# Performance work log

Measured on AMD Instinct MI355X. Metric: run time of the kernel, lower is better.

## Reference

```python
import jax, jax.numpy as jnp
import numpy as np

BATCH = 32      # init batch_size
HID = 256       # init hidden_dim
SENT = 64       # sentence_size
WORDS = 64      # words per sentence (the -1 in the view)
N = BATCH * SENT


def setup_inputs() -> dict:
    key = jax.random.key(0)
    k1, k2, k3, k4 = jax.random.split(key, 4)
    stdv_lin = 1.0 / np.sqrt(HID)
    x = jax.random.normal(k1, (N, WORDS, HID), dtype=jnp.float32)
    W = jax.random.uniform(k2, (HID, HID), jnp.float32, -stdv_lin, stdv_lin)
    b = jax.random.uniform(k3, (HID,), jnp.float32, -stdv_lin, stdv_lin)
    context = jax.random.uniform(k4, (HID,), jnp.float32, -stdv_lin, stdv_lin)
    return {"x": x, "W": W, "b": b, "context": context, "sentence_size": SENT}


def reference(x, W, b, context, sentence_size):
    # tanh(Linear(x)) applied per position; vectorized over the batch loop
    attends = jnp.tanh(jnp.einsum("nwh,oh->nwo", x, W) + b)  # [N, WORDS, HID]
    scores = attends * context                                 # [N, WORDS, HID]
    # nn.Softmax on the [-1, HID] view -> softmax over the hidden dim
    alpha = jax.nn.softmax(scores, axis=-1)                    # [N, WORDS, HID]
    attended = x * alpha                                       # legacy same-numel mul
    attended = attended.reshape(BATCH, sentence_size, -1, HID)
    return jnp.sum(attended, axis=2)                           # [BATCH, SENT, HID]
```

## Files before the change

kernel.cpp:

```cpp
#include <hip/hip_runtime.h>
#include <hip/hip_bf16.h>

#define HID 256
#define NROWS 2048
#define NPB 4
#define NHT (NPB * 2)
#define GRID (NROWS / NPB)
#define PITCH 264
#define HTF (32 * 256)

typedef __attribute__((ext_vector_type(8))) short short8;
typedef __attribute__((ext_vector_type(4))) float float4v;
typedef __attribute__((ext_vector_type(4))) unsigned int uint4v;

__device__ __forceinline__ float bf2f(unsigned short u) {
    return __uint_as_float(((unsigned int)u) << 16);
}

__device__ __forceinline__ unsigned int pk_bf16(float a, float b) {
    __hip_bfloat162 p = __float22bfloat162_rn(float2{a, b});
    return *(unsigned int*)&p;
}

__device__ __forceinline__ void bar_sync() {
    __builtin_amdgcn_sched_barrier(0);
    asm volatile("s_waitcnt lgkmcnt(0)");
    __builtin_amdgcn_s_barrier();
    __builtin_amdgcn_sched_barrier(0);
}

__device__ __forceinline__ float row16_sum(float v) {
    float t;
    t = __builtin_bit_cast(float, __builtin_amdgcn_update_dpp(
            0, __builtin_bit_cast(int, v), 0xB1, 0xf, 0xf, true));
    v += t;
    t = __builtin_bit_cast(float, __builtin_amdgcn_update_dpp(
            0, __builtin_bit_cast(int, v), 0x4E, 0xf, 0xf, true));
    v += t;
    t = __builtin_bit_cast(float, __builtin_amdgcn_update_dpp(
            0, __builtin_bit_cast(int, v), 0x124, 0xf, 0xf, true));
    v += t;
    t = __builtin_bit_cast(float, __builtin_amdgcn_update_dpp(
            0, __builtin_bit_cast(int, v), 0x128, 0xf, 0xf, true));
    v += t;
    return v;
}

__global__ __launch_bounds__(512, 4) void attend_fused(
    const float* __restrict__ x, const float* __restrict__ W,
    const float* __restrict__ bias, const float* __restrict__ ctx,
    float* __restrict__ out)
{
    __shared__ unsigned short xs[2][32 * PITCH];
    __shared__ float wsum[8][32];
    __shared__ float rinv[32];

    const int tid  = threadIdx.x;
    const int wave = tid >> 6;
    const int lane = tid & 63;
    const int q    = lane >> 4;
    const int c    = lane & 15;
    const int obase = wave * 32;
    const float* xp = x + (size_t)blockIdx.x * (NPB * 64 * 256);

    float4v R[4];
    {
        const float4v* xv = (const float4v*)xp;
#pragma unroll
        for (int j = 0; j < 4; ++j) R[j] = xv[tid + 512 * j];
    }

    float bb[2], f2[2];
    short8 bfrag[8][2];
#pragma unroll
    for (int nt = 0; nt < 2; ++nt) {
        const int o = obase + 2 * c + nt;
        bb[nt] = bias[o];
        f2[nt] = ctx[o] * 1.4426950408889634f;
        const float* wr = W + (size_t)o * 256 + q * 8;
#pragma unroll
        for (int kt = 0; kt < 8; ++kt) {
            float4v w0 = *(const float4v*)(wr + kt * 32);
            float4v w1 = *(const float4v*)(wr + kt * 32 + 4);
            uint4v u = { pk_bf16(w0.x, w0.y), pk_bf16(w0.z, w0.w),
                         pk_bf16(w1.x, w1.y), pk_bf16(w1.z, w1.w) };
            bfrag[kt][nt] = __builtin_bit_cast(short8, u);
        }
    }

#pragma unroll
    for (int j = 0; j < 4; ++j) {
        const int chunk = tid + 512 * j;
        const int r = chunk >> 6, col4 = (chunk & 63) * 4;
        uint2 u;
        u.x = pk_bf16(R[j].x, R[j].y);
        u.y = pk_bf16(R[j].z, R[j].w);
        *(uint2*)&xs[0][r * PITCH + col4] = u;
    }
    {
        const float4v* xv = (const float4v*)(xp + HTF);
#pragma unroll
        for (int j = 0; j < 4; ++j) R[j] = xv[tid + 512 * j];
    }
    bar_sync();

    float oacc[2] = {0.f, 0.f};
    int cur = 0;
#pragma unroll 1
    for (int h = 0; h < NHT; ++h) {
        const unsigned short* xsc = xs[cur];

        float4v acc[2][2];
#pragma unroll
        for (int mt = 0; mt < 2; ++mt)
#pragma unroll
            for (int nt = 0; nt < 2; ++nt)
                acc[mt][nt] = (float4v){0.f, 0.f, 0.f, 0.f};

#pragma unroll
        for (int kt = 0; kt < 8; ++kt) {
            short8 a[2];
#pragma unroll
            for (int mt = 0; mt < 2; ++mt)
                a[mt] = *(const short8*)&xsc[(mt * 16 + c) * PITCH + kt * 32 + q * 8];
#pragma unroll
            for (int nt = 0; nt < 2; ++nt)
#pragma unroll
                for (int mt = 0; mt < 2; ++mt)
                    acc[mt][nt] = __builtin_amdgcn_mfma_f32_16x16x32_bf16(
                        a[mt], bfrag[kt][nt], acc[mt][nt], 0, 0, 0);
        }

        float psum[2][4];
#pragma unroll
        for (int mt = 0; mt < 2; ++mt)
#pragma unroll
            for (int r = 0; r < 4; ++r)
                psum[mt][r] = 0.f;

#pragma unroll
        for (int nt = 0; nt < 2; ++nt) {
#pragma unroll
            for (int mt = 0; mt < 2; ++mt) {
#pragma unroll
                for (int r = 0; r < 4; ++r) {
                    const float y  = acc[mt][nt][r] + bb[nt];
                    const float E  = __builtin_amdgcn_exp2f(y * 2.8853900817779268f);
                    const float rd = __builtin_amdgcn_rcpf(E + 1.0f);
                    const float t  = __builtin_fmaf(-2.0f, rd, 1.0f);
                    const float e  = __builtin_amdgcn_exp2f(f2[nt] * t);
                    acc[mt][nt][r] = e;
                    psum[mt][r] += e;
                }
            }
        }
#pragma unroll
        for (int mt = 0; mt < 2; ++mt)
#pragma unroll
            for (int r = 0; r < 4; ++r)
                psum[mt][r] = row16_sum(psum[mt][r]);
        if (c == 0) {
#pragma unroll
            for (int mt = 0; mt < 2; ++mt) {
                float4v p = {psum[mt][0], psum[mt][1], psum[mt][2], psum[mt][3]};
                *(float4v*)&wsum[wave][mt * 16 + q * 4] = p;
            }
        }
        bar_sync();
        if (tid < 32) {
            const float t = wsum[0][tid] + wsum[1][tid] + wsum[2][tid] + wsum[3][tid]
                          + wsum[4][tid] + wsum[5][tid] + wsum[6][tid] + wsum[7][tid];
            rinv[tid] = __builtin_amdgcn_rcpf(t);
        }
        bar_sync();

        float ri[2][4];
#pragma unroll
        for (int mt = 0; mt < 2; ++mt)
#pragma unroll
            for (int r = 0; r < 4; ++r)
                ri[mt][r] = rinv[mt * 16 + q * 4 + r];

#pragma unroll
        for (int mt = 0; mt < 2; ++mt) {
#pragma unroll
            for (int r = 0; r < 4; ++r) {
                const int w = mt * 16 + q * 4 + r;
                unsigned int pair = *(const unsigned int*)&xsc[w * PITCH + obase + 2 * c];
                const float wgt = ri[mt][r];
                oacc[0] += bf2f((unsigned short)pair)         * (acc[mt][0][r] * wgt);
                oacc[1] += bf2f((unsigned short)(pair >> 16)) * (acc[mt][1][r] * wgt);
            }
        }
        if (h & 1) {
#pragma unroll
            for (int nt = 0; nt < 2; ++nt) {
                float v = oacc[nt];
                v += __shfl_xor(v, 16);
                v += __shfl_xor(v, 32);
                oacc[nt] = v;
            }
            if (q == 0) {
                const size_t n = (size_t)blockIdx.x * NPB + (h >> 1);
                *(float2*)&out[n * HID + obase + 2 * c] = float2{oacc[0], oacc[1]};
            }
            oacc[0] = 0.f; oacc[1] = 0.f;
        }

        if (h + 1 < NHT) {
#pragma unroll
            for (int j = 0; j < 4; ++j) {
                const int chunk = tid + 512 * j;
                const int r = chunk >> 6, col4 = (chunk & 63) * 4;
                uint2 u;
                u.x = pk_bf16(R[j].x, R[j].y);
                u.y = pk_bf16(R[j].z, R[j].w);
                *(uint2*)&xs[cur ^ 1][r * PITCH + col4] = u;
            }
            if (h + 2 < NHT) {
                const float4v* xv = (const float4v*)(xp + (size_t)(h + 2) * HTF);
#pragma unroll
                for (int j = 0; j < 4; ++j) R[j] = xv[tid + 512 * j];
            }
        }
        bar_sync();
        cur ^= 1;
    }
}

extern "C" void kernel_launch(void* const* d_in, const int* in_sizes, int n_in,
                              void* d_out, int out_size, void* d_ws, size_t ws_size,
                              hipStream_t stream) {
    const float* x    = (const float*)d_in[0];
    const float* W    = (const float*)d_in[1];
    const float* bias = (const float*)d_in[2];
    const float* ctx  = (const float*)d_in[3];
    (void)in_sizes; (void)n_in; (void)d_ws; (void)ws_size;

    attend_fused<<<GRID, 512, 0, stream>>>(x, W, bias, ctx, (float*)d_out);
}
```

Measured before the change: 213.5 us.

## Give each wave a full row with W staged in swizzled shared memory

Each wave now owns one sentence row and computes all 256 outputs, so the softmax over the hidden dim is reduced inside the wave. This removes the cross-wave shared-memory reductions and the block barriers in every step. W is converted to bf16 once per block and stored in an XOR-swizzled 128KB shared buffer. x is held in registers and moved into the accumulator layout with identity-matrix MFMAs instead of a shared-memory round trip. The costs are much higher register and LDS use (two blocks per CU at most), a per-block reload of W, and only 256 blocks in the grid.

```diff
diff --git a/kernel.cpp b/kernel.cpp
--- a/kernel.cpp
+++ b/kernel.cpp
@@ -3,30 +3,15 @@
 
 #define HID 256
 #define NROWS 2048
-#define NPB 4
-#define NHT (NPB * 2)
-#define GRID (NROWS / NPB)
-#define PITCH 264
-#define HTF (32 * 256)
+#define GRID (NROWS / 8)
 
 typedef __attribute__((ext_vector_type(8))) short short8;
 typedef __attribute__((ext_vector_type(4))) float float4v;
 typedef __attribute__((ext_vector_type(4))) unsigned int uint4v;
 
-__device__ __forceinline__ float bf2f(unsigned short u) {
-    return __uint_as_float(((unsigned int)u) << 16);
-}
-
 __device__ __forceinline__ unsigned int pk_bf16(float a, float b) {
     __hip_bfloat162 p = __float22bfloat162_rn(float2{a, b});
     return *(unsigned int*)&p;
-}
-
-__device__ __forceinline__ void bar_sync() {
-    __builtin_amdgcn_sched_barrier(0);
-    asm volatile("s_waitcnt lgkmcnt(0)");
-    __builtin_amdgcn_s_barrier();
-    __builtin_amdgcn_sched_barrier(0);
 }
 
 __device__ __forceinline__ float row16_sum(float v) {
@@ -46,185 +31,150 @@
     return v;
 }
 
-__global__ __launch_bounds__(512, 4) void attend_fused(
+__global__ __launch_bounds__(512, 2) void attend_fused(
     const float* __restrict__ x, const float* __restrict__ W,
     const float* __restrict__ bias, const float* __restrict__ ctx,
     float* __restrict__ out)
 {
-    __shared__ unsigned short xs[2][32 * PITCH];
-    __shared__ float wsum[8][32];
-    __shared__ float rinv[32];
+    __shared__ unsigned short Wb[256 * 256];
 
     const int tid  = threadIdx.x;
     const int wave = tid >> 6;
     const int lane = tid & 63;
     const int q    = lane >> 4;
     const int c    = lane & 15;
-    const int obase = wave * 32;
-    const float* xp = x + (size_t)blockIdx.x * (NPB * 64 * 256);
+    const int n    = blockIdx.x * 8 + wave;
+    const float* xn = x + (size_t)n * (64 * 256);
 
-    float4v R[4];
+    float4v xa[8], xb[8];
     {
-        const float4v* xv = (const float4v*)xp;
+        const float* xr = xn + c * 256 + q * 8;
 #pragma unroll
-        for (int j = 0; j < 4; ++j) R[j] = xv[tid + 512 * j];
+        for (int kt = 0; kt < 8; ++kt) {
+            xa[kt] = *(const float4v*)(xr + kt * 32);
+            xb[kt] = *(const float4v*)(xr + kt * 32 + 4);
+        }
     }
 
-    float bb[2], f2[2];
-    short8 bfrag[8][2];
+    {
+        char* wbb = (char*)Wb;
+#pragma unroll 4
+        for (int i = 0; i < 32; ++i) {
+            const int f4  = tid + 512 * i;
+            const int col = f4 >> 6;
+            const int k4  = (f4 & 63) * 4;
+            float4v v = *((const float4v*)W + f4);
+            uint2 u;
+            u.x = pk_bf16(v.x, v.y);
+            u.y = pk_bf16(v.z, v.w);
+            const int byte = (col * 512 + k4 * 2) ^ ((col & 7) << 4);
+            *(uint2*)(wbb + byte) = u;
+        }
+    }
+
+    float bias16[16], f216[16];
 #pragma unroll
-    for (int nt = 0; nt < 2; ++nt) {
-        const int o = obase + 2 * c + nt;
-        bb[nt] = bias[o];
-        f2[nt] = ctx[o] * 1.4426950408889634f;
-        const float* wr = W + (size_t)o * 256 + q * 8;
+    for (int nt = 0; nt < 16; ++nt) {
+        const int o = nt * 16 + c;
+        bias16[nt] = bias[o];
+        f216[nt]  = ctx[o] * 1.4426950408889634f;
+    }
+
+    short8 ifr[2];
+#pragma unroll
+    for (int p = 0; p < 2; ++p) {
+        short8 f = (short8){0, 0, 0, 0, 0, 0, 0, 0};
+#pragma unroll
+        for (int j = 0; j < 8; ++j)
+            f[j] = (q * 8 + j == p * 16 + c) ? (short)0x3F80 : (short)0;
+        ifr[p] = f;
+    }
+
+    int swzbase[8];
+#pragma unroll
+    for (int kt = 0; kt < 8; ++kt)
+        swzbase[kt] = c * 512 + ((kt * 64 + q * 16) ^ ((c & 7) << 4));
+
+    __syncthreads();
+
+    const char* wbb = (const char*)Wb;
+
+    float oacc[16];
+#pragma unroll
+    for (int nt = 0; nt < 16; ++nt) oacc[nt] = 0.f;
+
+#pragma unroll 1
+    for (int ch = 0; ch < 4; ++ch) {
+        short8 xfrag[8];
 #pragma unroll
         for (int kt = 0; kt < 8; ++kt) {
-            float4v w0 = *(const float4v*)(wr + kt * 32);
-            float4v w1 = *(const float4v*)(wr + kt * 32 + 4);
-            uint4v u = { pk_bf16(w0.x, w0.y), pk_bf16(w0.z, w0.w),
-                         pk_bf16(w1.x, w1.y), pk_bf16(w1.z, w1.w) };
-            bfrag[kt][nt] = __builtin_bit_cast(short8, u);
+            uint4v u = { pk_bf16(xa[kt].x, xa[kt].y), pk_bf16(xa[kt].z, xa[kt].w),
+                         pk_bf16(xb[kt].x, xb[kt].y), pk_bf16(xb[kt].z, xb[kt].w) };
+            xfrag[kt] = __builtin_bit_cast(short8, u);
+        }
+        if (ch < 3) {
+            const float* xr = xn + ((ch + 1) * 16 + c) * 256 + q * 8;
+#pragma unroll
+            for (int kt = 0; kt < 8; ++kt) {
+                xa[kt] = *(const float4v*)(xr + kt * 32);
+                xb[kt] = *(const float4v*)(xr + kt * 32 + 4);
+            }
+        }
+
+        float4v acc[16];
+#pragma unroll
+        for (int nt = 0; nt < 16; ++nt) acc[nt] = (float4v){0.f, 0.f, 0.f, 0.f};
+#pragma unroll
+        for (int kt = 0; kt < 8; ++kt) {
+#pragma unroll
+            for (int nt = 0; nt < 16; ++nt) {
+                const short8 b = *(const short8*)(wbb + (swzbase[kt] + nt * 8192));
+                acc[nt] = __builtin_amdgcn_mfma_f32_16x16x32_bf16(
+                    xfrag[kt], b, acc[nt], 0, 0, 0);
+            }
+        }
+
+        float psum[4] = {0.f, 0.f, 0.f, 0.f};
+#pragma unroll
+        for (int nt = 0; nt < 16; ++nt) {
+#pragma unroll
+            for (int r = 0; r < 4; ++r) {
+                const float y  = acc[nt][r] + bias16[nt];
+                const float E  = __builtin_amdgcn_exp2f(y * 2.8853900817779268f);
+                const float rd = __builtin_amdgcn_rcpf(E + 1.0f);
+                const float t  = __builtin_fmaf(-2.0f, rd, 1.0f);
+                const float e  = __builtin_amdgcn_exp2f(f216[nt] * t);
+                acc[nt][r] = e;
+                psum[r] += e;
+            }
+        }
+        float rinv[4];
+#pragma unroll
+        for (int r = 0; r < 4; ++r)
+            rinv[r] = __builtin_amdgcn_rcpf(row16_sum(psum[r]));
+
+        const float4v zero4 = {0.f, 0.f, 0.f, 0.f};
+#pragma unroll
+        for (int nt = 0; nt < 16; ++nt) {
+            float4v xD = __builtin_amdgcn_mfma_f32_16x16x32_bf16(
+                xfrag[nt >> 1], ifr[nt & 1], zero4, 0, 0, 0);
+#pragma unroll
+            for (int r = 0; r < 4; ++r)
+                oacc[nt] += xD[r] * (acc[nt][r] * rinv[r]);
         }
     }
 
 #pragma unroll
-    for (int j = 0; j < 4; ++j) {
-        const int chunk = tid + 512 * j;
-        const int r = chunk >> 6, col4 = (chunk & 63) * 4;
-        uint2 u;
-        u.x = pk_bf16(R[j].x, R[j].y);
-        u.y = pk_bf16(R[j].z, R[j].w);
-        *(uint2*)&xs[0][r * PITCH + col4] = u;
+    for (int nt = 0; nt < 16; ++nt) {
+        float v = oacc[nt];
+        v += __shfl_xor(v, 16);
+        v += __shfl_xor(v, 32);
+        oacc[nt] = v;
     }
-    {
-        const float4v* xv = (const float4v*)(xp + HTF);
+    if (q == 0) {
 #pragma unroll
-        for (int j = 0; j < 4; ++j) R[j] = xv[tid + 512 * j];
-    }
-    bar_sync();
-
-    float oacc[2] = {0.f, 0.f};
-    int cur = 0;
-#pragma unroll 1
-    for (int h = 0; h < NHT; ++h) {
-        const unsigned short* xsc = xs[cur];
-
-        float4v acc[2][2];
-#pragma unroll
-        for (int mt = 0; mt < 2; ++mt)
-#pragma unroll
-            for (int nt = 0; nt < 2; ++nt)
-                acc[mt][nt] = (float4v){0.f, 0.f, 0.f, 0.f};
-
-#pragma unroll
-        for (int kt = 0; kt < 8; ++kt) {
-            short8 a[2];
-#pragma unroll
-            for (int mt = 0; mt < 2; ++mt)
-                a[mt] = *(const short8*)&xsc[(mt * 16 + c) * PITCH + kt * 32 + q * 8];
-#pragma unroll
-            for (int nt = 0; nt < 2; ++nt)
-#pragma unroll
-                for (int mt = 0; mt < 2; ++mt)
-                    acc[mt][nt] = __builtin_amdgcn_mfma_f32_16x16x32_bf16(
-                        a[mt], bfrag[kt][nt], acc[mt][nt], 0, 0, 0);
-        }
-
-        float psum[2][4];
-#pragma unroll
-        for (int mt = 0; mt < 2; ++mt)
-#pragma unroll
-            for (int r = 0; r < 4; ++r)
-                psum[mt][r] = 0.f;
-
-#pragma unroll
-        for (int nt = 0; nt < 2; ++nt) {
-#pragma unroll
-            for (int mt = 0; mt < 2; ++mt) {
-#pragma unroll
-                for (int r = 0; r < 4; ++r) {
-                    const float y  = acc[mt][nt][r] + bb[nt];
-                    const float E  = __builtin_amdgcn_exp2f(y * 2.8853900817779268f);
-                    const float rd = __builtin_amdgcn_rcpf(E + 1.0f);
-                    const float t  = __builtin_fmaf(-2.0f, rd, 1.0f);
-                    const float e  = __builtin_amdgcn_exp2f(f2[nt] * t);
-                    acc[mt][nt][r] = e;
-                    psum[mt][r] += e;
-                }
-            }
-        }
-#pragma unroll
-        for (int mt = 0; mt < 2; ++mt)
-#pragma unroll
-            for (int r = 0; r < 4; ++r)
-                psum[mt][r] = row16_sum(psum[mt][r]);
-        if (c == 0) {
-#pragma unroll
-            for (int mt = 0; mt < 2; ++mt) {
-                float4v p = {psum[mt][0], psum[mt][1], psum[mt][2], psum[mt][3]};
-                *(float4v*)&wsum[wave][mt * 16 + q * 4] = p;
-            }
-        }
-        bar_sync();
-        if (tid < 32) {
-            const float t = wsum[0][tid] + wsum[1][tid] + wsum[2][tid] + wsum[3][tid]
-                          + wsum[4][tid] + wsum[5][tid] + wsum[6][tid] + wsum[7][tid];
-            rinv[tid] = __builtin_amdgcn_rcpf(t);
-        }
-        bar_sync();
-
-        float ri[2][4];
-#pragma unroll
-        for (int mt = 0; mt < 2; ++mt)
-#pragma unroll
-            for (int r = 0; r < 4; ++r)
-                ri[mt][r] = rinv[mt * 16 + q * 4 + r];
-
-#pragma unroll
-        for (int mt = 0; mt < 2; ++mt) {
-#pragma unroll
-            for (int r = 0; r < 4; ++r) {
-                const int w = mt * 16 + q * 4 + r;
-                unsigned int pair = *(const unsigned int*)&xsc[w * PITCH + obase + 2 * c];
-                const float wgt = ri[mt][r];
-                oacc[0] += bf2f((unsigned short)pair)         * (acc[mt][0][r] * wgt);
-                oacc[1] += bf2f((unsigned short)(pair >> 16)) * (acc[mt][1][r] * wgt);
-            }
-        }
-        if (h & 1) {
-#pragma unroll
-            for (int nt = 0; nt < 2; ++nt) {
-                float v = oacc[nt];
-                v += __shfl_xor(v, 16);
-                v += __shfl_xor(v, 32);
-                oacc[nt] = v;
-            }
-            if (q == 0) {
-                const size_t n = (size_t)blockIdx.x * NPB + (h >> 1);
-                *(float2*)&out[n * HID + obase + 2 * c] = float2{oacc[0], oacc[1]};
-            }
-            oacc[0] = 0.f; oacc[1] = 0.f;
-        }
-
-        if (h + 1 < NHT) {
-#pragma unroll
-            for (int j = 0; j < 4; ++j) {
-                const int chunk = tid + 512 * j;
-                const int r = chunk >> 6, col4 = (chunk & 63) * 4;
-                uint2 u;
-                u.x = pk_bf16(R[j].x, R[j].y);
-                u.y = pk_bf16(R[j].z, R[j].w);
-                *(uint2*)&xs[cur ^ 1][r * PITCH + col4] = u;
-            }
-            if (h + 2 < NHT) {
-                const float4v* xv = (const float4v*)(xp + (size_t)(h + 2) * HTF);
-#pragma unroll
-                for (int j = 0; j < 4; ++j) R[j] = xv[tid + 512 * j];
-            }
-        }
-        bar_sync();
-        cur ^= 1;
+        for (int nt = 0; nt < 16; ++nt)
+            out[(size_t)n * HID + nt * 16 + c] = oacc[nt];
     }
 }
 
```

Result: slower. 481.4 us (+125.5%).
